# Kernel optimization log

Measured on AMD Instinct MI355X. Metric: run time of the kernel, lower is better.

The kernel has to match this reference:

```python
import jax, jax.numpy as jnp
import numpy as np


def _soft_proto(x, P):
    d2 = (x * x).sum(-1, keepdims=True) - 2.0 * (x @ P.T) + (P * P).sum(-1)
    w = jax.nn.softmax(-d2, axis=-1)  # scores = -dist_sq, softmax over K
    return w @ P  # soft-matched prototypes


def setup_inputs() -> dict:
    key = jax.random.key(0)
    ks = jax.random.split(key, 12)
    B = 1024
    def u(k, shape, s=0.1):
        return jax.random.uniform(k, shape, minval=-s, maxval=s, dtype=jnp.float32)
    return {
        "fcn": jax.random.normal(ks[0], (B, 90, 90), jnp.float32),
        "scn": jax.random.normal(ks[1], (B, 90, 90), jnp.float32),
        # node embedding Linear(90->48), weights stored [in,out]
        "W_node": u(ks[2], (90, 48)), "b_node": jnp.zeros((48,), jnp.float32),
        "P_node": u(ks[3], (64, 48)),   # node prototypes, init uniform(-0.1,0.1)
        "W_graph": u(ks[4], (48, 32)), "b_graph": jnp.zeros((32,), jnp.float32),
        "P_graph": u(ks[5], (32, 32)),
        "Wg1": u(ks[6], (32, 32)), "bg1": jnp.zeros((32,), jnp.float32),
        "Wg2": u(ks[7], (32, 16)), "bg2": jnp.zeros((16,), jnp.float32),
        "P_cls": u(ks[8], (16, 16)),
        # classifier: final_dim = 2*90*48 + 2*32 + 2*16 = 8736
        "Wc1": u(ks[9], (8736, 256)), "bc1": jnp.zeros((256,), jnp.float32),
        "Wc2": u(ks[10], (256, 3)), "bc2": jnp.zeros((3,), jnp.float32),
    }


def reference(fcn, scn, W_node, b_node, P_node, W_graph, b_graph, P_graph,
              Wg1, bg1, Wg2, bg2, P_cls, Wc1, bc1, Wc2, bc2):
    def branch(x):
        nodes = x @ W_node + b_node                  # [B,90,48]
        nm = _soft_proto(nodes, P_node)              # [B,90,48]
        eg = nm.mean(axis=1) @ W_graph + b_graph     # [B,32]
        gp = _soft_proto(eg, P_graph)                # [B,32]
        ec = jax.nn.relu(gp @ Wg1 + bg1) @ Wg2 + bg2 # [B,16]
        cp = _soft_proto(ec, P_cls)                  # [B,16]
        return nm, gp, cp

    nmf, gpf, cpf = branch(fcn)
    nms, gps, cps = branch(scn)
    B = fcn.shape[0]
    R = jnp.concatenate(
        [nmf.reshape(B, -1), nms.reshape(B, -1), gpf, gps, cpf, cps], axis=-1)  # [B,8736]
    # dropout(0.5) is identity in eval mode
    logits = jax.nn.relu(R @ Wc1 + bc1) @ Wc2 + bc2  # [B,3]
    return logits
```

## Files before the change

### kernel.cpp

```cpp
#include <hip/hip_runtime.h>
#include <hip/hip_bf16.h>

using f16   = _Float16;
using f16x4 = __attribute__((ext_vector_type(4))) _Float16;
using f16x8 = __attribute__((ext_vector_type(8))) _Float16;
using f32x4 = __attribute__((ext_vector_type(4))) float;

__global__ __launch_bounds__(256) void prep_kernel(
    const float* __restrict__ Wn, const float* __restrict__ Pn,
    f16* __restrict__ wf, float* __restrict__ q)
{
  int i = blockIdx.x * 256 + threadIdx.x;
  if (i < 4992) {
    int n = i / 104, k = i - n * 104;
    wf[i] = (k < 90) ? (f16)Wn[k * 48 + n] : (f16)0.f;
  } else if (i < 8576) {
    int j = i - 4992; int p = j / 56, c = j - p * 56;
    wf[i] = (c < 48) ? (f16)Pn[p * 48 + c] : (f16)0.f;
  } else if (i < 12032) {
    int j = i - 8576; int r = j / 72, p = j - r * 72;
    wf[i] = (p < 64) ? (f16)Pn[p * 48 + r] : (f16)0.f;
  } else if (i < 12096) {
    int p = i - 12032;
    float s = 0.f;
    for (int j = 0; j < 48; ++j) { float v = Pn[p * 48 + j]; s = fmaf(v, v, s); }
    q[p] = s;
  }
}

__global__ __launch_bounds__(256) void wc1t_kernel(
    const float* __restrict__ Wc1, f16* __restrict__ Wc1T)
{
  __shared__ f16 sT[32 * 36];
  const int tid = threadIdx.x;
  const int kt = blockIdx.x, ct = blockIdx.y;
  const int c = tid & 31, r4 = (tid >> 5) * 4;
  #pragma unroll
  for (int i = 0; i < 4; ++i) {
    int r = r4 + i;
    sT[c * 36 + r] = (f16)Wc1[(size_t)(kt * 32 + r) * 256 + ct * 32 + c];
  }
  __syncthreads();
  #pragma unroll
  for (int i = 0; i < 4; ++i) {
    int r = r4 + i;
    Wc1T[(size_t)(ct * 32 + r) * 8736 + kt * 32 + c] = sT[r * 36 + c];
  }
}

__global__ __launch_bounds__(384) void node_kernel(
    const float* __restrict__ fcn, const float* __restrict__ scn,
    const float* __restrict__ bn, const f16* __restrict__ wf,
    const float* __restrict__ qg,
    f16* __restrict__ R, float* __restrict__ nmmean)
{
  __shared__ __align__(16) f16 sWt[12032];
  __shared__ __align__(16) f16 sS[6][1152];
  __shared__ float sCol[6][3][16];

  f16* sWnT = sWt;
  f16* sP   = sWt + 4992;
  f16* sPnT = sWt + 8576;

  const int tid = threadIdx.x;
  const int lane = tid & 63, wv = tid >> 6;
  const int l15 = lane & 15, lg = lane >> 4;
  const int b = blockIdx.x, br = blockIdx.y;
  const float* x = (br ? scn : fcn) + (size_t)b * 8100;
  f16* scr = sS[wv];

  for (int i = tid; i < 1504; i += 384)
    ((f16x8*)sWt)[i] = ((const f16x8*)wf)[i];
  __syncthreads();

  const int row = wv * 16 + l15;
  const float* xrow = x + row * 90;
  f16x8 a[3];
  #pragma unroll
  for (int kt = 0; kt < 3; ++kt) {
    const int k0 = kt * 32 + lg * 8;
    f16x8 h;
    #pragma unroll
    for (int e = 0; e < 8; ++e) h[e] = (f16)0.f;
    if (row < 90) {
      const float* src = xrow + k0;
      if (k0 < 88) {
        float2 u0 = *(const float2*)(src + 0);
        float2 u1 = *(const float2*)(src + 2);
        float2 u2 = *(const float2*)(src + 4);
        float2 u3 = *(const float2*)(src + 6);
        h[0] = (f16)u0.x; h[1] = (f16)u0.y; h[2] = (f16)u1.x; h[3] = (f16)u1.y;
        h[4] = (f16)u2.x; h[5] = (f16)u2.y; h[6] = (f16)u3.x; h[7] = (f16)u3.y;
      } else {
        float2 u0 = *(const float2*)src;
        h[0] = (f16)u0.x; h[1] = (f16)u0.y;
      }
    }
    a[kt] = h;
  }
  #pragma unroll
  for (int nt = 0; nt < 3; ++nt) {
    f32x4 acc = {0.f, 0.f, 0.f, 0.f};
    #pragma unroll
    for (int kt = 0; kt < 3; ++kt) {
      f16x8 bb = *(const f16x8*)&sWnT[(nt * 16 + l15) * 104 + kt * 32 + lg * 8];
      acc = __builtin_amdgcn_mfma_f32_16x16x32_f16(a[kt], bb, acc, 0, 0, 0);
    }
    const float bias = bn[nt * 16 + l15];
    #pragma unroll
    for (int r = 0; r < 4; ++r)
      scr[(lg * 4 + r) * 56 + nt * 16 + l15] = (f16)(acc[r] + bias);
  }
  asm volatile("s_waitcnt lgkmcnt(0)" ::: "memory");
  __builtin_amdgcn_sched_barrier(0);

  const f16x8 a0 = *(const f16x8*)&scr[l15 * 56 + lg * 8];
  const f16x4 a1 = *(const f16x4*)&scr[l15 * 56 + 32 + lg * 4];
  f32x4 acc2[4];
  #pragma unroll
  for (int nt = 0; nt < 4; ++nt) acc2[nt] = (f32x4){0.f, 0.f, 0.f, 0.f};
  #pragma unroll
  for (int nt = 0; nt < 4; ++nt) {
    f16x8 b0 = *(const f16x8*)&sP[(nt * 16 + l15) * 56 + lg * 8];
    acc2[nt] = __builtin_amdgcn_mfma_f32_16x16x32_f16(a0, b0, acc2[nt], 0, 0, 0);
    f16x4 b1 = *(const f16x4*)&sP[(nt * 16 + l15) * 56 + 32 + lg * 4];
    acc2[nt] = __builtin_amdgcn_mfma_f32_16x16x16f16(a1, b1, acc2[nt], 0, 0, 0);
  }
  float qv[4];
  #pragma unroll
  for (int nt = 0; nt < 4; ++nt) qv[nt] = qg[nt * 16 + l15];
  #pragma unroll
  for (int r = 0; r < 4; ++r) {
    float s0 = 2.f * acc2[0][r] - qv[0];
    float s1 = 2.f * acc2[1][r] - qv[1];
    float s2 = 2.f * acc2[2][r] - qv[2];
    float s3 = 2.f * acc2[3][r] - qv[3];
    float m = fmaxf(fmaxf(s0, s1), fmaxf(s2, s3));
    m = fmaxf(m, __shfl_xor(m, 1, 64));
    m = fmaxf(m, __shfl_xor(m, 2, 64));
    m = fmaxf(m, __shfl_xor(m, 4, 64));
    m = fmaxf(m, __shfl_xor(m, 8, 64));
    float e0 = __expf(s0 - m), e1 = __expf(s1 - m);
    float e2 = __expf(s2 - m), e3 = __expf(s3 - m);
    float sum = (e0 + e1) + (e2 + e3);
    sum += __shfl_xor(sum, 1, 64);
    sum += __shfl_xor(sum, 2, 64);
    sum += __shfl_xor(sum, 4, 64);
    sum += __shfl_xor(sum, 8, 64);
    const float inv = 1.f / sum;
    const int lr = lg * 4 + r;
    scr[lr * 72 + 0 * 16 + l15] = (f16)(e0 * inv);
    scr[lr * 72 + 1 * 16 + l15] = (f16)(e1 * inv);
    scr[lr * 72 + 2 * 16 + l15] = (f16)(e2 * inv);
    scr[lr * 72 + 3 * 16 + l15] = (f16)(e3 * inv);
  }
  asm volatile("s_waitcnt lgkmcnt(0)" ::: "memory");
  __builtin_amdgcn_sched_barrier(0);

  f16* Rrow = R + (size_t)b * 8736 + (size_t)br * 4320;
  const f16x8 wa0 = *(const f16x8*)&scr[l15 * 72 + lg * 8];
  const f16x8 wa1 = *(const f16x8*)&scr[l15 * 72 + 32 + lg * 8];
  float cs[3] = {0.f, 0.f, 0.f};
  #pragma unroll
  for (int nt = 0; nt < 3; ++nt) {
    f32x4 acc = {0.f, 0.f, 0.f, 0.f};
    f16x8 b0 = *(const f16x8*)&sPnT[(nt * 16 + l15) * 72 + lg * 8];
    acc = __builtin_amdgcn_mfma_f32_16x16x32_f16(wa0, b0, acc, 0, 0, 0);
    f16x8 b1 = *(const f16x8*)&sPnT[(nt * 16 + l15) * 72 + 32 + lg * 8];
    acc = __builtin_amdgcn_mfma_f32_16x16x32_f16(wa1, b1, acc, 0, 0, 0);
    #pragma unroll
    for (int r = 0; r < 4; ++r) {
      const int grow = wv * 16 + lg * 4 + r;
      if (grow < 90) {
        Rrow[grow * 48 + nt * 16 + l15] = (f16)acc[r];
        cs[nt] += acc[r];
      }
    }
  }
  #pragma unroll
  for (int nt = 0; nt < 3; ++nt) {
    cs[nt] += __shfl_xor(cs[nt], 16, 64);
    cs[nt] += __shfl_xor(cs[nt], 32, 64);
  }
  if (lane < 16) {
    sCol[wv][0][lane] = cs[0];
    sCol[wv][1][lane] = cs[1];
    sCol[wv][2][lane] = cs[2];
  }
  __syncthreads();
  if (tid < 48) {
    const int nt = tid >> 4, c = tid & 15;
    float s = 0.f;
    #pragma unroll
    for (int w = 0; w < 6; ++w) s += sCol[w][nt][c];
    nmmean[((size_t)br * 1024 + b) * 48 + tid] = s * (1.f / 90.f);
  }
}

__global__ __launch_bounds__(256) void graph_kernel(
    const float* __restrict__ nmmean,
    const float* __restrict__ Wg, const float* __restrict__ bg,
    const float* __restrict__ Pg,
    const float* __restrict__ Wg1, const float* __restrict__ bg1,
    const float* __restrict__ Wg2, const float* __restrict__ bg2,
    const float* __restrict__ Pc,
    f16* __restrict__ R)
{
  __shared__ float sE[4][64];
  __shared__ float sT[4][64];
  const int tid = threadIdx.x;
  const int wid = tid >> 6, lane = tid & 63;
  const int idx = blockIdx.x * 4 + wid;
  const int br = idx >> 10, b = idx & 1023;
  const float* mrow = nmmean + (size_t)idx * 48;
  f16* Rrow = R + (size_t)b * 8736;

  if (lane < 32) {
    float e = bg[lane];
    #pragma unroll
    for (int k = 0; k < 48; ++k) e = fmaf(mrow[k], Wg[k * 32 + lane], e);
    sE[wid][lane] = e;
  }
  __syncthreads();
  if (lane < 32) {
    float s = 0.f;
    #pragma unroll
    for (int j = 0; j < 32; ++j) { float pv = Pg[lane * 32 + j]; s += pv * (2.f * sE[wid][j] - pv); }
    float m = s;
    for (int d = 16; d >= 1; d >>= 1) m = fmaxf(m, __shfl_xor(m, d, 64));
    float ex = __expf(s - m);
    float sum = ex;
    for (int d = 16; d >= 1; d >>= 1) sum += __shfl_xor(sum, d, 64);
    sT[wid][lane] = ex / sum;
  }
  __syncthreads();
  if (lane < 32) {
    float g = 0.f;
    #pragma unroll
    for (int p = 0; p < 32; ++p) g = fmaf(sT[wid][p], Pg[p * 32 + lane], g);
    Rrow[8640 + br * 32 + lane] = (f16)g;
    sE[wid][lane] = g;
  }
  __syncthreads();
  if (lane < 32) {
    float h = bg1[lane];
    #pragma unroll
    for (int k = 0; k < 32; ++k) h = fmaf(sE[wid][k], Wg1[k * 32 + lane], h);
    sT[wid][lane] = fmaxf(h, 0.f);
  }
  __syncthreads();
  if (lane < 16) {
    float c = bg2[lane];
    #pragma unroll
    for (int k = 0; k < 32; ++k) c = fmaf(sT[wid][k], Wg2[k * 16 + lane], c);
    sE[wid][lane] = c;
  }
  __syncthreads();
  if (lane < 16) {
    float s = 0.f;
    #pragma unroll
    for (int j = 0; j < 16; ++j) { float pv = Pc[lane * 16 + j]; s += pv * (2.f * sE[wid][j] - pv); }
    float m = s;
    for (int d = 8; d >= 1; d >>= 1) m = fmaxf(m, __shfl_xor(m, d, 64));
    float ex = __expf(s - m);
    float sum = ex;
    for (int d = 8; d >= 1; d >>= 1) sum += __shfl_xor(sum, d, 64);
    sT[wid][lane] = ex / sum;
  }
  __syncthreads();
  if (lane < 16) {
    float c = 0.f;
    #pragma unroll
    for (int p = 0; p < 16; ++p) c = fmaf(sT[wid][p], Pc[p * 16 + lane], c);
    Rrow[8704 + br * 16 + lane] = (f16)c;
  }
}

__global__ __launch_bounds__(256) void gemm1_kernel(
    const f16* __restrict__ R, const f16* __restrict__ Wc1T,
    float* __restrict__ part, int KS)
{
  __shared__ __align__(16) f16 sA[128 * 40];
  __shared__ __align__(16) f16 sB[64 * 40];
  const int tid = threadIdx.x;
  const int lane = tid & 63, wv = tid >> 6;
  const int l15 = lane & 15, lg = lane >> 4;
  const int wm = wv >> 1, wn = wv & 1;
  const int bm = blockIdx.x * 128, bnc = blockIdx.y * 64, z = blockIdx.z;
  const int base = 273 / KS, rem = 273 - base * KS;
  const int t0 = z * base + (z < rem ? z : rem);
  const int nt_ = base + (z < rem ? 1 : 0);
  const int kbeg = t0 * 32, kend = (t0 + nt_) * 32;

  const int ar = tid >> 1, ah = (tid & 1) * 16;
  const int bc = tid >> 2, bh = (tid & 3) * 8;

  f32x4 acc[4][2];
  #pragma unroll
  for (int mt = 0; mt < 4; ++mt)
    #pragma unroll
    for (int nt = 0; nt < 2; ++nt) acc[mt][nt] = (f32x4){0.f, 0.f, 0.f, 0.f};

  f16x8 v0 = *(const f16x8*)&R[(size_t)(bm + ar) * 8736 + kbeg + ah];
  f16x8 v1 = *(const f16x8*)&R[(size_t)(bm + ar) * 8736 + kbeg + ah + 8];
  f16x8 w0 = *(const f16x8*)&Wc1T[(size_t)(bnc + bc) * 8736 + kbeg + bh];

  for (int kk = kbeg; kk < kend; kk += 32) {
    *(f16x8*)&sA[ar * 40 + ah] = v0;
    *(f16x8*)&sA[ar * 40 + ah + 8] = v1;
    *(f16x8*)&sB[bc * 40 + bh] = w0;
    __syncthreads();
    if (kk + 32 < kend) {
      v0 = *(const f16x8*)&R[(size_t)(bm + ar) * 8736 + kk + 32 + ah];
      v1 = *(const f16x8*)&R[(size_t)(bm + ar) * 8736 + kk + 32 + ah + 8];
      w0 = *(const f16x8*)&Wc1T[(size_t)(bnc + bc) * 8736 + kk + 32 + bh];
    }
    #pragma unroll
    for (int mt = 0; mt < 4; ++mt) {
      f16x8 a = *(const f16x8*)&sA[(wm * 64 + mt * 16 + l15) * 40 + lg * 8];
      #pragma unroll
      for (int nt = 0; nt < 2; ++nt) {
        f16x8 bb = *(const f16x8*)&sB[(wn * 32 + nt * 16 + l15) * 40 + lg * 8];
        acc[mt][nt] = __builtin_amdgcn_mfma_f32_16x16x32_f16(a, bb, acc[mt][nt], 0, 0, 0);
      }
    }
    __syncthreads();
  }
  float* pz = part + (size_t)z * 262144;
  #pragma unroll
  for (int mt = 0; mt < 4; ++mt)
    #pragma unroll
    for (int nt = 0; nt < 2; ++nt)
      #pragma unroll
      for (int r = 0; r < 4; ++r)
        pz[(size_t)(bm + wm * 64 + mt * 16 + lg * 4 + r) * 256 +
           bnc + wn * 32 + nt * 16 + l15] = acc[mt][nt][r];
}

__global__ __launch_bounds__(256) void head_kernel(
    const float* __restrict__ part, const float* __restrict__ bc1,
    const float* __restrict__ Wc2, const float* __restrict__ bc2,
    float* __restrict__ out, int KS)
{
  __shared__ float red[3][4];
  const int b = blockIdx.x, t = threadIdx.x;
  float s0 = 0.f, s1 = 0.f, s2 = 0.f, s3 = 0.f;
  int z = 0;
  for (; z + 4 <= KS; z += 4) {
    s0 += part[(size_t)(z + 0) * 262144 + (size_t)b * 256 + t];
    s1 += part[(size_t)(z + 1) * 262144 + (size_t)b * 256 + t];
    s2 += part[(size_t)(z + 2) * 262144 + (size_t)b * 256 + t];
    s3 += part[(size_t)(z + 3) * 262144 + (size_t)b * 256 + t];
  }
  for (; z < KS; ++z) s0 += part[(size_t)z * 262144 + (size_t)b * 256 + t];
  float acc = bc1[t] + ((s0 + s1) + (s2 + s3));
  float h = fmaxf(acc, 0.f);
  float p0 = h * Wc2[t * 3 + 0];
  float p1 = h * Wc2[t * 3 + 1];
  float p2 = h * Wc2[t * 3 + 2];
  for (int d = 32; d >= 1; d >>= 1) {
    p0 += __shfl_xor(p0, d, 64);
    p1 += __shfl_xor(p1, d, 64);
    p2 += __shfl_xor(p2, d, 64);
  }
  const int wid = t >> 6, lane = t & 63;
  if (lane == 0) { red[0][wid] = p0; red[1][wid] = p1; red[2][wid] = p2; }
  __syncthreads();
  if (t < 3) {
    out[(size_t)b * 3 + t] = red[t][0] + red[t][1] + red[t][2] + red[t][3] + bc2[t];
  }
}

extern "C" void kernel_launch(void* const* d_in, const int* in_sizes, int n_in,
                              void* d_out, int out_size, void* d_ws, size_t ws_size,
                              hipStream_t stream) {
  const float* fcn     = (const float*)d_in[0];
  const float* scn     = (const float*)d_in[1];
  const float* W_node  = (const float*)d_in[2];
  const float* b_node  = (const float*)d_in[3];
  const float* P_node  = (const float*)d_in[4];
  const float* W_graph = (const float*)d_in[5];
  const float* b_graph = (const float*)d_in[6];
  const float* P_graph = (const float*)d_in[7];
  const float* Wg1     = (const float*)d_in[8];
  const float* bg1     = (const float*)d_in[9];
  const float* Wg2     = (const float*)d_in[10];
  const float* bg2     = (const float*)d_in[11];
  const float* P_cls   = (const float*)d_in[12];
  const float* Wc1     = (const float*)d_in[13];
  const float* bc1     = (const float*)d_in[14];
  const float* Wc2     = (const float*)d_in[15];
  const float* bc2     = (const float*)d_in[16];
  float* out = (float*)d_out;

  char* ws = (char*)d_ws;
  f16*   R16    = (f16*)ws;
  f16*   Wc1T   = (f16*)(ws + 17891328);
  f16*   wf     = (f16*)(ws + 22364160);
  float* qbuf   = (float*)(ws + 22388224);
  float* nmmean = (float*)(ws + 22388480);
  float* part   = (float*)(ws + 22781696);

  size_t avail = ws_size > 22781696u ? ws_size - 22781696u : 0;
  int KS = (int)(avail / 1048576u);
  if (KS > 16) KS = 16;
  if (KS < 1) KS = 1;

  prep_kernel<<<48, 256, 0, stream>>>(W_node, P_node, wf, qbuf);
  wc1t_kernel<<<dim3(273, 8), 256, 0, stream>>>(Wc1, Wc1T);
  node_kernel<<<dim3(1024, 2), 384, 0, stream>>>(fcn, scn, b_node, wf, qbuf,
                                                 R16, nmmean);
  graph_kernel<<<512, 256, 0, stream>>>(nmmean, W_graph, b_graph, P_graph,
                                        Wg1, bg1, Wg2, bg2, P_cls, R16);
  gemm1_kernel<<<dim3(8, 4, KS), 256, 0, stream>>>(R16, Wc1T, part, KS);
  head_kernel<<<1024, 256, 0, stream>>>(part, bc1, Wc2, bc2, out, KS);
}
```

Measured before the change: 67.85 us.

## Process two samples per node_kernel block to amortize weight staging

Each node_kernel block now handles two (branch, batch) samples instead of one, halving the grid to 1024 blocks. The shared-memory weight staging (about 24 KB copied per block) is amortized over two samples, and the B-fragment LDS reads are reused across both samples' MFMAs, with the two independent MFMA chains interleaved for ILP. In exchange, shared memory and register use per block roughly double, which may lower occupancy, and there are fewer blocks to spread across CUs. The nmmean index is still consistent because u = bx*2+s maps onto br*1024+b.

```diff
diff --git a/kernel.cpp b/kernel.cpp
--- a/kernel.cpp
+++ b/kernel.cpp
@@ -55,8 +55,8 @@
     f16* __restrict__ R, float* __restrict__ nmmean)
 {
   __shared__ __align__(16) f16 sWt[12032];
-  __shared__ __align__(16) f16 sS[6][1152];
-  __shared__ float sCol[6][3][16];
+  __shared__ __align__(16) f16 sS[6][2][1152];
+  __shared__ float sCol[6][2][3][16];
 
   f16* sWnT = sWt;
   f16* sP   = sWt + 4992;
@@ -65,135 +65,177 @@
   const int tid = threadIdx.x;
   const int lane = tid & 63, wv = tid >> 6;
   const int l15 = lane & 15, lg = lane >> 4;
-  const int b = blockIdx.x, br = blockIdx.y;
-  const float* x = (br ? scn : fcn) + (size_t)b * 8100;
-  f16* scr = sS[wv];
+  const int bx = blockIdx.x;
+
+  const float* xs[2];
+  f16* Rr[2];
+  #pragma unroll
+  for (int s = 0; s < 2; ++s) {
+    const int u = bx * 2 + s;
+    const int br = u >> 10, b = u & 1023;
+    xs[s] = (br ? scn : fcn) + (size_t)b * 8100;
+    Rr[s] = R + (size_t)b * 8736 + (size_t)br * 4320;
+  }
 
   for (int i = tid; i < 1504; i += 384)
     ((f16x8*)sWt)[i] = ((const f16x8*)wf)[i];
   __syncthreads();
 
   const int row = wv * 16 + l15;
-  const float* xrow = x + row * 90;
-  f16x8 a[3];
-  #pragma unroll
-  for (int kt = 0; kt < 3; ++kt) {
-    const int k0 = kt * 32 + lg * 8;
-    f16x8 h;
-    #pragma unroll
-    for (int e = 0; e < 8; ++e) h[e] = (f16)0.f;
-    if (row < 90) {
-      const float* src = xrow + k0;
-      if (k0 < 88) {
-        float2 u0 = *(const float2*)(src + 0);
-        float2 u1 = *(const float2*)(src + 2);
-        float2 u2 = *(const float2*)(src + 4);
-        float2 u3 = *(const float2*)(src + 6);
-        h[0] = (f16)u0.x; h[1] = (f16)u0.y; h[2] = (f16)u1.x; h[3] = (f16)u1.y;
-        h[4] = (f16)u2.x; h[5] = (f16)u2.y; h[6] = (f16)u3.x; h[7] = (f16)u3.y;
-      } else {
-        float2 u0 = *(const float2*)src;
-        h[0] = (f16)u0.x; h[1] = (f16)u0.y;
+  f16x8 a[2][3];
+  #pragma unroll
+  for (int s = 0; s < 2; ++s) {
+    const float* xrow = xs[s] + row * 90;
+    #pragma unroll
+    for (int kt = 0; kt < 3; ++kt) {
+      const int k0 = kt * 32 + lg * 8;
+      f16x8 h;
+      #pragma unroll
+      for (int e = 0; e < 8; ++e) h[e] = (f16)0.f;
+      if (row < 90) {
+        const float* src = xrow + k0;
+        if (k0 < 88) {
+          float2 u0 = *(const float2*)(src + 0);
+          float2 u1 = *(const float2*)(src + 2);
+          float2 u2 = *(const float2*)(src + 4);
+          float2 u3 = *(const float2*)(src + 6);
+          h[0] = (f16)u0.x; h[1] = (f16)u0.y; h[2] = (f16)u1.x; h[3] = (f16)u1.y;
+          h[4] = (f16)u2.x; h[5] = (f16)u2.y; h[6] = (f16)u3.x; h[7] = (f16)u3.y;
+        } else {
+          float2 u0 = *(const float2*)src;
+          h[0] = (f16)u0.x; h[1] = (f16)u0.y;
+        }
       }
-    }
-    a[kt] = h;
-  }
+      a[s][kt] = h;
+    }
+  }
+
+  f32x4 acc1[2][3];
+  #pragma unroll
+  for (int s = 0; s < 2; ++s)
+    #pragma unroll
+    for (int nt = 0; nt < 3; ++nt) acc1[s][nt] = (f32x4){0.f, 0.f, 0.f, 0.f};
   #pragma unroll
   for (int nt = 0; nt < 3; ++nt) {
-    f32x4 acc = {0.f, 0.f, 0.f, 0.f};
     #pragma unroll
     for (int kt = 0; kt < 3; ++kt) {
       f16x8 bb = *(const f16x8*)&sWnT[(nt * 16 + l15) * 104 + kt * 32 + lg * 8];
-      acc = __builtin_amdgcn_mfma_f32_16x16x32_f16(a[kt], bb, acc, 0, 0, 0);
+      #pragma unroll
+      for (int s = 0; s < 2; ++s)
+        acc1[s][nt] = __builtin_amdgcn_mfma_f32_16x16x32_f16(a[s][kt], bb, acc1[s][nt], 0, 0, 0);
     }
     const float bias = bn[nt * 16 + l15];
     #pragma unroll
-    for (int r = 0; r < 4; ++r)
-      scr[(lg * 4 + r) * 56 + nt * 16 + l15] = (f16)(acc[r] + bias);
+    for (int s = 0; s < 2; ++s)
+      #pragma unroll
+      for (int r = 0; r < 4; ++r)
+        sS[wv][s][(lg * 4 + r) * 56 + nt * 16 + l15] = (f16)(acc1[s][nt][r] + bias);
   }
   asm volatile("s_waitcnt lgkmcnt(0)" ::: "memory");
   __builtin_amdgcn_sched_barrier(0);
 
-  const f16x8 a0 = *(const f16x8*)&scr[l15 * 56 + lg * 8];
-  const f16x4 a1 = *(const f16x4*)&scr[l15 * 56 + 32 + lg * 4];
-  f32x4 acc2[4];
-  #pragma unroll
-  for (int nt = 0; nt < 4; ++nt) acc2[nt] = (f32x4){0.f, 0.f, 0.f, 0.f};
+  f16x8 a0[2]; f16x4 a1[2];
+  #pragma unroll
+  for (int s = 0; s < 2; ++s) {
+    a0[s] = *(const f16x8*)&sS[wv][s][l15 * 56 + lg * 8];
+    a1[s] = *(const f16x4*)&sS[wv][s][l15 * 56 + 32 + lg * 4];
+  }
+  f32x4 acc2[2][4];
+  #pragma unroll
+  for (int s = 0; s < 2; ++s)
+    #pragma unroll
+    for (int nt = 0; nt < 4; ++nt) acc2[s][nt] = (f32x4){0.f, 0.f, 0.f, 0.f};
   #pragma unroll
   for (int nt = 0; nt < 4; ++nt) {
     f16x8 b0 = *(const f16x8*)&sP[(nt * 16 + l15) * 56 + lg * 8];
-    acc2[nt] = __builtin_amdgcn_mfma_f32_16x16x32_f16(a0, b0, acc2[nt], 0, 0, 0);
     f16x4 b1 = *(const f16x4*)&sP[(nt * 16 + l15) * 56 + 32 + lg * 4];
-    acc2[nt] = __builtin_amdgcn_mfma_f32_16x16x16f16(a1, b1, acc2[nt], 0, 0, 0);
+    #pragma unroll
+    for (int s = 0; s < 2; ++s) {
+      acc2[s][nt] = __builtin_amdgcn_mfma_f32_16x16x32_f16(a0[s], b0, acc2[s][nt], 0, 0, 0);
+      acc2[s][nt] = __builtin_amdgcn_mfma_f32_16x16x16f16(a1[s], b1, acc2[s][nt], 0, 0, 0);
+    }
   }
   float qv[4];
   #pragma unroll
   for (int nt = 0; nt < 4; ++nt) qv[nt] = qg[nt * 16 + l15];
   #pragma unroll
-  for (int r = 0; r < 4; ++r) {
-    float s0 = 2.f * acc2[0][r] - qv[0];
-    float s1 = 2.f * acc2[1][r] - qv[1];
-    float s2 = 2.f * acc2[2][r] - qv[2];
-    float s3 = 2.f * acc2[3][r] - qv[3];
-    float m = fmaxf(fmaxf(s0, s1), fmaxf(s2, s3));
-    m = fmaxf(m, __shfl_xor(m, 1, 64));
-    m = fmaxf(m, __shfl_xor(m, 2, 64));
-    m = fmaxf(m, __shfl_xor(m, 4, 64));
-    m = fmaxf(m, __shfl_xor(m, 8, 64));
-    float e0 = __expf(s0 - m), e1 = __expf(s1 - m);
-    float e2 = __expf(s2 - m), e3 = __expf(s3 - m);
-    float sum = (e0 + e1) + (e2 + e3);
-    sum += __shfl_xor(sum, 1, 64);
-    sum += __shfl_xor(sum, 2, 64);
-    sum += __shfl_xor(sum, 4, 64);
-    sum += __shfl_xor(sum, 8, 64);
-    const float inv = 1.f / sum;
-    const int lr = lg * 4 + r;
-    scr[lr * 72 + 0 * 16 + l15] = (f16)(e0 * inv);
-    scr[lr * 72 + 1 * 16 + l15] = (f16)(e1 * inv);
-    scr[lr * 72 + 2 * 16 + l15] = (f16)(e2 * inv);
-    scr[lr * 72 + 3 * 16 + l15] = (f16)(e3 * inv);
+  for (int s = 0; s < 2; ++s) {
+    #pragma unroll
+    for (int r = 0; r < 4; ++r) {
+      float s0 = 2.f * acc2[s][0][r] - qv[0];
+      float s1 = 2.f * acc2[s][1][r] - qv[1];
+      float s2 = 2.f * acc2[s][2][r] - qv[2];
+      float s3 = 2.f * acc2[s][3][r] - qv[3];
+      float m = fmaxf(fmaxf(s0, s1), fmaxf(s2, s3));
+      m = fmaxf(m, __shfl_xor(m, 1, 64));
+      m = fmaxf(m, __shfl_xor(m, 2, 64));
+      m = fmaxf(m, __shfl_xor(m, 4, 64));
+      m = fmaxf(m, __shfl_xor(m, 8, 64));
+      float e0 = __expf(s0 - m), e1 = __expf(s1 - m);
+      float e2 = __expf(s2 - m), e3 = __expf(s3 - m);
+      float sum = (e0 + e1) + (e2 + e3);
+      sum += __shfl_xor(sum, 1, 64);
+      sum += __shfl_xor(sum, 2, 64);
+      sum += __shfl_xor(sum, 4, 64);
+      sum += __shfl_xor(sum, 8, 64);
+      const float inv = 1.f / sum;
+      const int lr = lg * 4 + r;
+      sS[wv][s][lr * 72 + 0 * 16 + l15] = (f16)(e0 * inv);
+      sS[wv][s][lr * 72 + 1 * 16 + l15] = (f16)(e1 * inv);
+      sS[wv][s][lr * 72 + 2 * 16 + l15] = (f16)(e2 * inv);
+      sS[wv][s][lr * 72 + 3 * 16 + l15] = (f16)(e3 * inv);
+    }
   }
   asm volatile("s_waitcnt lgkmcnt(0)" ::: "memory");
   __builtin_amdgcn_sched_barrier(0);
 
-  f16* Rrow = R + (size_t)b * 8736 + (size_t)br * 4320;
-  const f16x8 wa0 = *(const f16x8*)&scr[l15 * 72 + lg * 8];
-  const f16x8 wa1 = *(const f16x8*)&scr[l15 * 72 + 32 + lg * 8];
-  float cs[3] = {0.f, 0.f, 0.f};
+  f16x8 wa0[2], wa1[2];
+  #pragma unroll
+  for (int s = 0; s < 2; ++s) {
+    wa0[s] = *(const f16x8*)&sS[wv][s][l15 * 72 + lg * 8];
+    wa1[s] = *(const f16x8*)&sS[wv][s][l15 * 72 + 32 + lg * 8];
+  }
+  float cs[2][3] = {{0.f, 0.f, 0.f}, {0.f, 0.f, 0.f}};
   #pragma unroll
   for (int nt = 0; nt < 3; ++nt) {
-    f32x4 acc = {0.f, 0.f, 0.f, 0.f};
     f16x8 b0 = *(const f16x8*)&sPnT[(nt * 16 + l15) * 72 + lg * 8];
-    acc = __builtin_amdgcn_mfma_f32_16x16x32_f16(wa0, b0, acc, 0, 0, 0);
     f16x8 b1 = *(const f16x8*)&sPnT[(nt * 16 + l15) * 72 + 32 + lg * 8];
-    acc = __builtin_amdgcn_mfma_f32_16x16x32_f16(wa1, b1, acc, 0, 0, 0);
-    #pragma unroll
-    for (int r = 0; r < 4; ++r) {
-      const int grow = wv * 16 + lg * 4 + r;
-      if (grow < 90) {
-        Rrow[grow * 48 + nt * 16 + l15] = (f16)acc[r];
-        cs[nt] += acc[r];
+    #pragma unroll
+    for (int s = 0; s < 2; ++s) {
+      f32x4 acc = {0.f, 0.f, 0.f, 0.f};
+      acc = __builtin_amdgcn_mfma_f32_16x16x32_f16(wa0[s], b0, acc, 0, 0, 0);
+      acc = __builtin_amdgcn_mfma_f32_16x16x32_f16(wa1[s], b1, acc, 0, 0, 0);
+      #pragma unroll
+      for (int r = 0; r < 4; ++r) {
+        const int grow = wv * 16 + lg * 4 + r;
+        if (grow < 90) {
+          Rr[s][grow * 48 + nt * 16 + l15] = (f16)acc[r];
+          cs[s][nt] += acc[r];
+        }
       }
     }
   }
   #pragma unroll
-  for (int nt = 0; nt < 3; ++nt) {
-    cs[nt] += __shfl_xor(cs[nt], 16, 64);
-    cs[nt] += __shfl_xor(cs[nt], 32, 64);
-  }
+  for (int s = 0; s < 2; ++s)
+    #pragma unroll
+    for (int nt = 0; nt < 3; ++nt) {
+      cs[s][nt] += __shfl_xor(cs[s][nt], 16, 64);
+      cs[s][nt] += __shfl_xor(cs[s][nt], 32, 64);
+    }
   if (lane < 16) {
-    sCol[wv][0][lane] = cs[0];
-    sCol[wv][1][lane] = cs[1];
-    sCol[wv][2][lane] = cs[2];
-  }
-  __syncthreads();
-  if (tid < 48) {
-    const int nt = tid >> 4, c = tid & 15;
-    float s = 0.f;
-    #pragma unroll
-    for (int w = 0; w < 6; ++w) s += sCol[w][nt][c];
-    nmmean[((size_t)br * 1024 + b) * 48 + tid] = s * (1.f / 90.f);
+    #pragma unroll
+    for (int s = 0; s < 2; ++s)
+      #pragma unroll
+      for (int nt = 0; nt < 3; ++nt) sCol[wv][s][nt][lane] = cs[s][nt];
+  }
+  __syncthreads();
+  if (tid < 96) {
+    const int s = tid / 48, c48 = tid - s * 48;
+    const int nt = c48 >> 4, c = c48 & 15;
+    float sum = 0.f;
+    #pragma unroll
+    for (int w = 0; w < 6; ++w) sum += sCol[w][s][nt][c];
+    nmmean[(size_t)(bx * 2 + s) * 48 + c48] = sum * (1.f / 90.f);
   }
 }
 
@@ -408,8 +450,8 @@
 
   prep_kernel<<<48, 256, 0, stream>>>(W_node, P_node, wf, qbuf);
   wc1t_kernel<<<dim3(273, 8), 256, 0, stream>>>(Wc1, Wc1T);
-  node_kernel<<<dim3(1024, 2), 384, 0, stream>>>(fcn, scn, b_node, wf, qbuf,
-                                                 R16, nmmean);
+  node_kernel<<<1024, 384, 0, stream>>>(fcn, scn, b_node, wf, qbuf,
+                                        R16, nmmean);
   graph_kernel<<<512, 256, 0, stream>>>(nmmean, W_graph, b_graph, P_graph,
                                         Wg1, bg1, Wg2, bg2, P_cls, R16);
   gemm1_kernel<<<dim3(8, 4, KS), 256, 0, stream>>>(R16, Wc1T, part, KS);
```

Result: slower. 69.24 us (+2.0%).

## Fuse graph branch into head kernel and merge prep launches

Applied to the files above, without the earlier changes.

Merges the two preprocessing kernels into one launch and removes the separate graph kernel. The graph/class prototype computation now runs inside the head kernel, and its 96 output features are multiplied by the fp32 Wc1 tail rows directly. The split-K GEMM therefore covers only the first 8640 columns of R. This drops two kernel launches and the f16 round trip for the tail features, but adds serial per-row work to each head block and leaves the wc1t transpose and prep work in a single launch.

```diff
diff --git a/kernel.cpp b/kernel.cpp
--- a/kernel.cpp
+++ b/kernel.cpp
@@ -6,45 +6,46 @@
 using f16x8 = __attribute__((ext_vector_type(8))) _Float16;
 using f32x4 = __attribute__((ext_vector_type(4))) float;
 
-__global__ __launch_bounds__(256) void prep_kernel(
+__global__ __launch_bounds__(256) void prepwc1t_kernel(
+    const float* __restrict__ Wc1, f16* __restrict__ Wc1T,
     const float* __restrict__ Wn, const float* __restrict__ Pn,
     f16* __restrict__ wf, float* __restrict__ q)
 {
-  int i = blockIdx.x * 256 + threadIdx.x;
-  if (i < 4992) {
-    int n = i / 104, k = i - n * 104;
-    wf[i] = (k < 90) ? (f16)Wn[k * 48 + n] : (f16)0.f;
-  } else if (i < 8576) {
-    int j = i - 4992; int p = j / 56, c = j - p * 56;
-    wf[i] = (c < 48) ? (f16)Pn[p * 48 + c] : (f16)0.f;
-  } else if (i < 12032) {
-    int j = i - 8576; int r = j / 72, p = j - r * 72;
-    wf[i] = (p < 64) ? (f16)Pn[p * 48 + r] : (f16)0.f;
-  } else if (i < 12096) {
-    int p = i - 12032;
-    float s = 0.f;
-    for (int j = 0; j < 48; ++j) { float v = Pn[p * 48 + j]; s = fmaf(v, v, s); }
-    q[p] = s;
-  }
-}
-
-__global__ __launch_bounds__(256) void wc1t_kernel(
-    const float* __restrict__ Wc1, f16* __restrict__ Wc1T)
-{
-  __shared__ f16 sT[32 * 36];
+  const int blk = blockIdx.x;
   const int tid = threadIdx.x;
-  const int kt = blockIdx.x, ct = blockIdx.y;
-  const int c = tid & 31, r4 = (tid >> 5) * 4;
-  #pragma unroll
-  for (int i = 0; i < 4; ++i) {
-    int r = r4 + i;
-    sT[c * 36 + r] = (f16)Wc1[(size_t)(kt * 32 + r) * 256 + ct * 32 + c];
-  }
-  __syncthreads();
-  #pragma unroll
-  for (int i = 0; i < 4; ++i) {
-    int r = r4 + i;
-    Wc1T[(size_t)(ct * 32 + r) * 8736 + kt * 32 + c] = sT[r * 36 + c];
+  if (blk < 2184) {
+    __shared__ f16 sT[32 * 36];
+    const int kt = blk % 273, ct = blk / 273;
+    const int c = tid & 31, r4 = (tid >> 5) * 4;
+    #pragma unroll
+    for (int i = 0; i < 4; ++i) {
+      int r = r4 + i;
+      sT[c * 36 + r] = (f16)Wc1[(size_t)(kt * 32 + r) * 256 + ct * 32 + c];
+    }
+    __syncthreads();
+    #pragma unroll
+    for (int i = 0; i < 4; ++i) {
+      int r = r4 + i;
+      Wc1T[(size_t)(ct * 32 + r) * 8736 + kt * 32 + c] = sT[r * 36 + c];
+    }
+  } else {
+    for (int i = tid; i < 12096; i += 256) {
+      if (i < 4992) {
+        int n = i / 104, k = i - n * 104;
+        wf[i] = (k < 90) ? (f16)Wn[k * 48 + n] : (f16)0.f;
+      } else if (i < 8576) {
+        int j = i - 4992; int p = j / 56, c2 = j - p * 56;
+        wf[i] = (c2 < 48) ? (f16)Pn[p * 48 + c2] : (f16)0.f;
+      } else if (i < 12032) {
+        int j = i - 8576; int r = j / 72, p = j - r * 72;
+        wf[i] = (p < 64) ? (f16)Pn[p * 48 + r] : (f16)0.f;
+      } else {
+        int p = i - 12032;
+        float s = 0.f;
+        for (int j = 0; j < 48; ++j) { float v = Pn[p * 48 + j]; s = fmaf(v, v, s); }
+        q[p] = s;
+      }
+    }
   }
 }
 
@@ -197,85 +198,6 @@
   }
 }
 
-__global__ __launch_bounds__(256) void graph_kernel(
-    const float* __restrict__ nmmean,
-    const float* __restrict__ Wg, const float* __restrict__ bg,
-    const float* __restrict__ Pg,
-    const float* __restrict__ Wg1, const float* __restrict__ bg1,
-    const float* __restrict__ Wg2, const float* __restrict__ bg2,
-    const float* __restrict__ Pc,
-    f16* __restrict__ R)
-{
-  __shared__ float sE[4][64];
-  __shared__ float sT[4][64];
-  const int tid = threadIdx.x;
-  const int wid = tid >> 6, lane = tid & 63;
-  const int idx = blockIdx.x * 4 + wid;
-  const int br = idx >> 10, b = idx & 1023;
-  const float* mrow = nmmean + (size_t)idx * 48;
-  f16* Rrow = R + (size_t)b * 8736;
-
-  if (lane < 32) {
-    float e = bg[lane];
-    #pragma unroll
-    for (int k = 0; k < 48; ++k) e = fmaf(mrow[k], Wg[k * 32 + lane], e);
-    sE[wid][lane] = e;
-  }
-  __syncthreads();
-  if (lane < 32) {
-    float s = 0.f;
-    #pragma unroll
-    for (int j = 0; j < 32; ++j) { float pv = Pg[lane * 32 + j]; s += pv * (2.f * sE[wid][j] - pv); }
-    float m = s;
-    for (int d = 16; d >= 1; d >>= 1) m = fmaxf(m, __shfl_xor(m, d, 64));
-    float ex = __expf(s - m);
-    float sum = ex;
-    for (int d = 16; d >= 1; d >>= 1) sum += __shfl_xor(sum, d, 64);
-    sT[wid][lane] = ex / sum;
-  }
-  __syncthreads();
-  if (lane < 32) {
-    float g = 0.f;
-    #pragma unroll
-    for (int p = 0; p < 32; ++p) g = fmaf(sT[wid][p], Pg[p * 32 + lane], g);
-    Rrow[8640 + br * 32 + lane] = (f16)g;
-    sE[wid][lane] = g;
-  }
-  __syncthreads();
-  if (lane < 32) {
-    float h = bg1[lane];
-    #pragma unroll
-    for (int k = 0; k < 32; ++k) h = fmaf(sE[wid][k], Wg1[k * 32 + lane], h);
-    sT[wid][lane] = fmaxf(h, 0.f);
-  }
-  __syncthreads();
-  if (lane < 16) {
-    float c = bg2[lane];
-    #pragma unroll
-    for (int k = 0; k < 32; ++k) c = fmaf(sT[wid][k], Wg2[k * 16 + lane], c);
-    sE[wid][lane] = c;
-  }
-  __syncthreads();
-  if (lane < 16) {
-    float s = 0.f;
-    #pragma unroll
-    for (int j = 0; j < 16; ++j) { float pv = Pc[lane * 16 + j]; s += pv * (2.f * sE[wid][j] - pv); }
-    float m = s;
-    for (int d = 8; d >= 1; d >>= 1) m = fmaxf(m, __shfl_xor(m, d, 64));
-    float ex = __expf(s - m);
-    float sum = ex;
-    for (int d = 8; d >= 1; d >>= 1) sum += __shfl_xor(sum, d, 64);
-    sT[wid][lane] = ex / sum;
-  }
-  __syncthreads();
-  if (lane < 16) {
-    float c = 0.f;
-    #pragma unroll
-    for (int p = 0; p < 16; ++p) c = fmaf(sT[wid][p], Pc[p * 16 + lane], c);
-    Rrow[8704 + br * 16 + lane] = (f16)c;
-  }
-}
-
 __global__ __launch_bounds__(256) void gemm1_kernel(
     const f16* __restrict__ R, const f16* __restrict__ Wc1T,
     float* __restrict__ part, int KS)
@@ -287,7 +209,7 @@
   const int l15 = lane & 15, lg = lane >> 4;
   const int wm = wv >> 1, wn = wv & 1;
   const int bm = blockIdx.x * 128, bnc = blockIdx.y * 64, z = blockIdx.z;
-  const int base = 273 / KS, rem = 273 - base * KS;
+  const int base = 270 / KS, rem = 270 - base * KS;
   const int t0 = z * base + (z < rem ? z : rem);
   const int nt_ = base + (z < rem ? 1 : 0);
   const int kbeg = t0 * 32, kend = (t0 + nt_) * 32;
@@ -338,12 +260,24 @@
 }
 
 __global__ __launch_bounds__(256) void head_kernel(
-    const float* __restrict__ part, const float* __restrict__ bc1,
+    const float* __restrict__ part, const float* __restrict__ nmmean,
+    const float* __restrict__ Wg, const float* __restrict__ bg,
+    const float* __restrict__ Pg,
+    const float* __restrict__ Wg1, const float* __restrict__ bg1,
+    const float* __restrict__ Wg2, const float* __restrict__ bg2,
+    const float* __restrict__ Pc,
+    const float* __restrict__ Wc1, const float* __restrict__ bc1,
     const float* __restrict__ Wc2, const float* __restrict__ bc2,
     float* __restrict__ out, int KS)
 {
+  __shared__ float sG[2][32];
+  __shared__ float sC[2][16];
+  __shared__ float sE[2][32];
+  __shared__ float sT[2][32];
   __shared__ float red[3][4];
   const int b = blockIdx.x, t = threadIdx.x;
+  const int wid = t >> 6, lane = t & 63;
+
   float s0 = 0.f, s1 = 0.f, s2 = 0.f, s3 = 0.f;
   int z = 0;
   for (; z + 4 <= KS; z += 4) {
@@ -353,7 +287,91 @@
     s3 += part[(size_t)(z + 3) * 262144 + (size_t)b * 256 + t];
   }
   for (; z < KS; ++z) s0 += part[(size_t)z * 262144 + (size_t)b * 256 + t];
-  float acc = bc1[t] + ((s0 + s1) + (s2 + s3));
+  float s_part = (s0 + s1) + (s2 + s3);
+
+  if (wid < 2) {
+    const float* mrow = nmmean + (size_t)(wid * 1024 + b) * 48;
+    if (lane < 32) {
+      float e = bg[lane];
+      #pragma unroll
+      for (int k = 0; k < 48; ++k) e = fmaf(mrow[k], Wg[k * 32 + lane], e);
+      sE[wid][lane] = e;
+    }
+    asm volatile("s_waitcnt lgkmcnt(0)" ::: "memory");
+    __builtin_amdgcn_sched_barrier(0);
+    if (lane < 32) {
+      float s = 0.f;
+      #pragma unroll
+      for (int j = 0; j < 32; ++j) { float pv = Pg[lane * 32 + j]; s += pv * (2.f * sE[wid][j] - pv); }
+      float m = s;
+      for (int d = 16; d >= 1; d >>= 1) m = fmaxf(m, __shfl_xor(m, d, 64));
+      float ex = __expf(s - m);
+      float sum = ex;
+      for (int d = 16; d >= 1; d >>= 1) sum += __shfl_xor(sum, d, 64);
+      sT[wid][lane] = ex / sum;
+    }
+    asm volatile("s_waitcnt lgkmcnt(0)" ::: "memory");
+    __builtin_amdgcn_sched_barrier(0);
+    if (lane < 32) {
+      float g = 0.f;
+      #pragma unroll
+      for (int p = 0; p < 32; ++p) g = fmaf(sT[wid][p], Pg[p * 32 + lane], g);
+      sG[wid][lane] = g;
+    }
+    asm volatile("s_waitcnt lgkmcnt(0)" ::: "memory");
+    __builtin_amdgcn_sched_barrier(0);
+    if (lane < 32) {
+      float h = bg1[lane];
+      #pragma unroll
+      for (int k = 0; k < 32; ++k) h = fmaf(sG[wid][k], Wg1[k * 32 + lane], h);
+      sT[wid][lane] = fmaxf(h, 0.f);
+    }
+    asm volatile("s_waitcnt lgkmcnt(0)" ::: "memory");
+    __builtin_amdgcn_sched_barrier(0);
+    if (lane < 16) {
+      float c = bg2[lane];
+      #pragma unroll
+      for (int k = 0; k < 32; ++k) c = fmaf(sT[wid][k], Wg2[k * 16 + lane], c);
+      sE[wid][lane] = c;
+    }
+    asm volatile("s_waitcnt lgkmcnt(0)" ::: "memory");
+    __builtin_amdgcn_sched_barrier(0);
+    if (lane < 16) {
+      float s = 0.f;
+      #pragma unroll
+      for (int j = 0; j < 16; ++j) { float pv = Pc[lane * 16 + j]; s += pv * (2.f * sE[wid][j] - pv); }
+      float m = s;
+      for (int d = 8; d >= 1; d >>= 1) m = fmaxf(m, __shfl_xor(m, d, 64));
+      float ex = __expf(s - m);
+      float sum = ex;
+      for (int d = 8; d >= 1; d >>= 1) sum += __shfl_xor(sum, d, 64);
+      sT[wid][lane] = ex / sum;
+    }
+    asm volatile("s_waitcnt lgkmcnt(0)" ::: "memory");
+    __builtin_amdgcn_sched_barrier(0);
+    if (lane < 16) {
+      float c = 0.f;
+      #pragma unroll
+      for (int p = 0; p < 16; ++p) c = fmaf(sT[wid][p], Pc[p * 16 + lane], c);
+      sC[wid][lane] = c;
+    }
+  }
+  __syncthreads();
+
+  float acc = bc1[t] + s_part;
+  #pragma unroll 8
+  for (int k = 0; k < 32; ++k)
+    acc = fmaf(sG[0][k], Wc1[(size_t)(8640 + k) * 256 + t], acc);
+  #pragma unroll 8
+  for (int k = 0; k < 32; ++k)
+    acc = fmaf(sG[1][k], Wc1[(size_t)(8672 + k) * 256 + t], acc);
+  #pragma unroll 8
+  for (int k = 0; k < 16; ++k)
+    acc = fmaf(sC[0][k], Wc1[(size_t)(8704 + k) * 256 + t], acc);
+  #pragma unroll 8
+  for (int k = 0; k < 16; ++k)
+    acc = fmaf(sC[1][k], Wc1[(size_t)(8720 + k) * 256 + t], acc);
+
   float h = fmaxf(acc, 0.f);
   float p0 = h * Wc2[t * 3 + 0];
   float p1 = h * Wc2[t * 3 + 1];
@@ -363,7 +381,6 @@
     p1 += __shfl_xor(p1, d, 64);
     p2 += __shfl_xor(p2, d, 64);
   }
-  const int wid = t >> 6, lane = t & 63;
   if (lane == 0) { red[0][wid] = p0; red[1][wid] = p1; red[2][wid] = p2; }
   __syncthreads();
   if (t < 3) {
@@ -406,12 +423,11 @@
   if (KS > 16) KS = 16;
   if (KS < 1) KS = 1;
 
-  prep_kernel<<<48, 256, 0, stream>>>(W_node, P_node, wf, qbuf);
-  wc1t_kernel<<<dim3(273, 8), 256, 0, stream>>>(Wc1, Wc1T);
+  prepwc1t_kernel<<<2185, 256, 0, stream>>>(Wc1, Wc1T, W_node, P_node, wf, qbuf);
   node_kernel<<<dim3(1024, 2), 384, 0, stream>>>(fcn, scn, b_node, wf, qbuf,
                                                  R16, nmmean);
-  graph_kernel<<<512, 256, 0, stream>>>(nmmean, W_graph, b_graph, P_graph,
-                                        Wg1, bg1, Wg2, bg2, P_cls, R16);
   gemm1_kernel<<<dim3(8, 4, KS), 256, 0, stream>>>(R16, Wc1T, part, KS);
-  head_kernel<<<1024, 256, 0, stream>>>(part, bc1, Wc2, bc2, out, KS);
+  head_kernel<<<1024, 256, 0, stream>>>(part, nmmean, W_graph, b_graph, P_graph,
+                                        Wg1, bg1, Wg2, bg2, P_cls,
+                                        Wc1, bc1, Wc2, bc2, out, KS);
 }
```

Result: slower. 76.87 us (+13.3%).
